# Performance work log

Measured on AMD Instinct MI355X. Metric: run time of the kernel, lower is better.

The kernel has to match this reference:

```python
import jax, jax.numpy as jnp
import numpy as np
from jax import lax

N = 25600      # total nodes = G * T
E = 204800     # edges (before self loops)
IN_CH = 6
HID = 64
HEADS = 4
G = 512        # graphs per batch
T = 50         # sequence length (node_time in [0, T))
OUT = 30       # prediction_horizon * 3
NEG_SLOPE = 0.2
BN_EPS = 1e-5


def _gat(x, src, dst, W, a_src, a_dst, b, heads, outc):
    # PyG GATConv (concat=True): h = x W reshaped to (N, H, C)
    n = x.shape[0]
    h = (x @ W).reshape(n, heads, outc)
    # edge scores: leaky_relu(a_src . h_src + a_dst . h_dst), softmax over incoming edges of dst
    e = jax.nn.leaky_relu((h * a_src).sum(-1)[src] + (h * a_dst).sum(-1)[dst], NEG_SLOPE)  # (E, H)
    m = jax.ops.segment_max(e, dst, num_segments=n)
    ex = jnp.exp(e - m[dst])
    denom = jax.ops.segment_sum(ex, dst, num_segments=n)
    alpha = ex / denom[dst]
    out = jax.ops.segment_sum(alpha[:, :, None] * h[src], dst, num_segments=n)  # (N, H, C)
    return out.reshape(n, heads * outc) + b


def _bn_eval(x, g, b):
    # BatchNorm in eval with running_mean=0, running_var=1
    return g * (x * (1.0 / np.float32(np.sqrt(1.0 + BN_EPS)))) + b


def setup_inputs() -> dict:
    ks = jax.random.split(jax.random.key(0), 16)
    s = 0.1
    d = {}
    d["x"] = jax.random.normal(ks[0], (N, IN_CH), jnp.float32)
    d["edge_index"] = jax.random.randint(ks[1], (2, E), 0, N)
    idx = jnp.arange(N)
    d["batch"] = idx // T       # each graph has exactly T nodes
    d["node_time"] = idx % T
    d["W1"] = jax.random.normal(ks[2], (IN_CH, HEADS * HID), jnp.float32) * s
    d["att_src1"] = jax.random.normal(ks[3], (HEADS, HID), jnp.float32) * s
    d["att_dst1"] = jax.random.normal(ks[4], (HEADS, HID), jnp.float32) * s
    d["b1"] = jnp.zeros((HEADS * HID,), jnp.float32)
    d["g1"] = jnp.ones((HEADS * HID,), jnp.float32)
    d["be1"] = jnp.zeros((HEADS * HID,), jnp.float32)
    d["W2"] = jax.random.normal(ks[5], (HEADS * HID, HID), jnp.float32) * s
    d["att_src2"] = jax.random.normal(ks[6], (1, HID), jnp.float32) * s
    d["att_dst2"] = jax.random.normal(ks[7], (1, HID), jnp.float32) * s
    d["b2"] = jnp.zeros((HID,), jnp.float32)
    d["g2"] = jnp.ones((HID,), jnp.float32)
    d["be2"] = jnp.zeros((HID,), jnp.float32)
    d["Wih"] = jax.random.normal(ks[8], (4 * HID, HID), jnp.float32) * s
    d["Whh"] = jax.random.normal(ks[9], (4 * HID, HID), jnp.float32) * s
    d["bih"] = jnp.zeros((4 * HID,), jnp.float32)
    d["bhh"] = jnp.zeros((4 * HID,), jnp.float32)
    d["Wfc"] = jax.random.normal(ks[10], (HID, OUT), jnp.float32) * s
    d["bfc"] = jnp.zeros((OUT,), jnp.float32)
    return d


def reference(x, edge_index, batch, node_time, W1, att_src1, att_dst1, b1, g1, be1,
              W2, att_src2, att_dst2, b2, g2, be2, Wih, Whh, bih, bhh, Wfc, bfc):
    loops = jnp.arange(N)
    src = jnp.concatenate([edge_index[0], loops])  # GATConv adds self loops
    dst = jnp.concatenate([edge_index[1], loops])
    h = jax.nn.elu(_bn_eval(_gat(x, src, dst, W1, att_src1, att_dst1, b1, HEADS, HID), g1, be1))
    h = jax.nn.elu(_bn_eval(_gat(h, src, dst, W2, att_src2, att_dst2, b2, 1, HID), g2, be2))
    # vectorized replacement of the per-node python scatter loop
    x_seq = jnp.zeros((G, T, HID), h.dtype).at[batch, node_time].set(h)

    def step(carry, xt):
        hh, cc = carry
        gates = xt @ Wih.T + bih + hh @ Whh.T + bhh
        i, f, gg, o = jnp.split(gates, 4, axis=-1)
        cc = jax.nn.sigmoid(f) * cc + jax.nn.sigmoid(i) * jnp.tanh(gg)
        hh = jax.nn.sigmoid(o) * jnp.tanh(cc)
        return (hh, cc), None

    init = (jnp.zeros((G, HID), h.dtype), jnp.zeros((G, HID), h.dtype))
    (hn, _), _ = lax.scan(step, init, x_seq.transpose(1, 0, 2))  # scan over time
    return hn @ Wfc + bfc  # (G, 30)
```

## Files before the change

### kernel.cpp

```cpp
#include <hip/hip_runtime.h>

#define N_NODES 25600
#define N_EDGES 204800
#define EE (N_EDGES + N_NODES)
#define IN_CH 6
#define HID 64
#define HEADS 4
#define G_GRAPHS 512
#define T_STEPS 50
#define OUT_DIM 30
#define NEG_SLOPE 0.2f
#define BN_INV 0.9999950000374997f

__device__ __forceinline__ float lrelu_(float x){ return x > 0.f ? x : NEG_SLOPE * x; }
__device__ __forceinline__ float elu_(float x){ return x > 0.f ? x : __expf(x) - 1.f; }
__device__ __forceinline__ float sigmoid_(float x){ return 1.f / (1.f + __expf(-x)); }

__global__ void count_k(const int* __restrict__ ei, int* __restrict__ counts){
    int e = blockIdx.x * 256 + threadIdx.x;
    if (e >= EE) return;
    int dst = (e < N_EDGES) ? ei[N_EDGES + e] : (e - N_EDGES);
    atomicAdd(&counts[dst], 1);
}

__global__ void scan_k(const int* __restrict__ counts, int* __restrict__ row_ptr,
                       int* __restrict__ cursor){
    __shared__ int part[1024];
    int t = threadIdx.x;
    const int CH = N_NODES / 1024;
    int base = t * CH;
    int s = 0;
    for (int i = 0; i < CH; i++) s += counts[base + i];
    part[t] = s;
    __syncthreads();
    for (int off = 1; off < 1024; off <<= 1){
        int v = (t >= off) ? part[t - off] : 0;
        __syncthreads();
        part[t] += v;
        __syncthreads();
    }
    int run = (t > 0) ? part[t - 1] : 0;
    for (int i = 0; i < CH; i++){
        int cv = counts[base + i];
        row_ptr[base + i] = run;
        cursor[base + i]  = run;
        run += cv;
    }
    if (t == 1023) row_ptr[N_NODES] = run;
}

__global__ void scatter_k(const int* __restrict__ ei, int* __restrict__ cursor,
                          int* __restrict__ ssrc){
    int e = blockIdx.x * 256 + threadIdx.x;
    if (e >= EE) return;
    int src, dst;
    if (e < N_EDGES){ src = ei[e]; dst = ei[N_EDGES + e]; }
    else            { src = dst = e - N_EDGES; }
    int pos = atomicAdd(&cursor[dst], 1);
    ssrc[pos] = src;
}

__global__ void gat1_tr(const float* __restrict__ x, const float* __restrict__ W1,
                        const float* __restrict__ asw, const float* __restrict__ adw,
                        float* __restrict__ h1_pre, float* __restrict__ as1,
                        float* __restrict__ ad1){
    __shared__ float w[IN_CH * 256];
    int tid = threadIdx.x;
    for (int i = tid; i < IN_CH * 256; i += 256) w[i] = W1[i];
    __syncthreads();
    int wv = tid >> 6, lane = tid & 63;
    int n = blockIdx.x * 4 + wv;
    float xv[IN_CH];
    #pragma unroll
    for (int k = 0; k < IN_CH; k++) xv[k] = x[n * IN_CH + k];
    float sA[4], sD[4];
    #pragma unroll
    for (int h = 0; h < 4; h++){
        int col = h * 64 + lane;
        float acc = 0.f;
        #pragma unroll
        for (int k = 0; k < IN_CH; k++) acc += xv[k] * w[k * 256 + col];
        h1_pre[n * 256 + col] = acc;
        sA[h] = acc * asw[col];
        sD[h] = acc * adw[col];
    }
    #pragma unroll
    for (int h = 0; h < 4; h++){
        #pragma unroll
        for (int off = 32; off; off >>= 1){
            sA[h] += __shfl_xor(sA[h], off);
            sD[h] += __shfl_xor(sD[h], off);
        }
    }
    if (lane == 0){
        *(float4*)&as1[n * 4] = make_float4(sA[0], sA[1], sA[2], sA[3]);
        *(float4*)&ad1[n * 4] = make_float4(sD[0], sD[1], sD[2], sD[3]);
    }
}

__global__ void gat1_agg(const float* __restrict__ h1_pre, const float* __restrict__ as1,
                         const float* __restrict__ ad1, const int* __restrict__ row_ptr,
                         const int* __restrict__ ssrc,
                         const float* __restrict__ b1, const float* __restrict__ g1,
                         const float* __restrict__ be1, float* __restrict__ h1_act){
    int wv = threadIdx.x >> 6, lane = threadIdx.x & 63;
    int n = blockIdx.x * 4 + wv;
    int s0 = row_ptr[n], s1 = row_ptr[n + 1];
    float4 adn = *(const float4*)&ad1[n * 4];
    float d0 = 0.f, d1 = 0.f, d2 = 0.f, d3 = 0.f;
    float a0 = 0.f, a1 = 0.f, a2 = 0.f, a3 = 0.f;
    for (int j = s0; j < s1; j++){
        int s = ssrc[j];
        float4 as = *(const float4*)&as1[s * 4];
        float e0 = __expf(lrelu_(as.x + adn.x));
        float e1 = __expf(lrelu_(as.y + adn.y));
        float e2 = __expf(lrelu_(as.z + adn.z));
        float e3 = __expf(lrelu_(as.w + adn.w));
        d0 += e0; d1 += e1; d2 += e2; d3 += e3;
        const float* hp = h1_pre + (size_t)s * 256;
        a0 += e0 * hp[lane];
        a1 += e1 * hp[64 + lane];
        a2 += e2 * hp[128 + lane];
        a3 += e3 * hp[192 + lane];
    }
    float accs[4] = {a0 / d0, a1 / d1, a2 / d2, a3 / d3};
    #pragma unroll
    for (int h = 0; h < 4; h++){
        int col = h * 64 + lane;
        float v = accs[h] + b1[col];
        v = g1[col] * (v * BN_INV) + be1[col];
        h1_act[(size_t)n * 256 + col] = elu_(v);
    }
}

#define TM 64
#define KT 32
#define APAD 4
__global__ __launch_bounds__(256) void gat2_tr(const float* __restrict__ h1_act,
                        const float* __restrict__ W2,
                        const float* __restrict__ asw, const float* __restrict__ adw,
                        float* __restrict__ h2_pre, float* __restrict__ as2,
                        float* __restrict__ ad2){
    __shared__ float As[TM][KT + APAD];
    __shared__ float Bs[KT][64];
    int tx = threadIdx.x;
    int rg = tx >> 4;
    int cg = tx & 15;
    int r0 = rg * 4, c0 = cg * 4;
    int rowBase = blockIdx.x * TM;
    float acc[4][4] = {};
    for (int k0 = 0; k0 < 256; k0 += KT){
        #pragma unroll
        for (int it = 0; it < 2; it++){
            int i = tx + it * 256;
            int row = i >> 3;
            int c4  = (i & 7) * 4;
            *(float4*)&As[row][c4] =
                *(const float4*)(h1_act + (size_t)(rowBase + row) * 256 + k0 + c4);
        }
        #pragma unroll
        for (int it = 0; it < 2; it++){
            int i = tx + it * 256;
            int row = i >> 4;
            int c4  = (i & 15) * 4;
            *(float4*)&Bs[row][c4] = *(const float4*)(W2 + (size_t)(k0 + row) * 64 + c4);
        }
        __syncthreads();
        #pragma unroll
        for (int kq = 0; kq < KT; kq += 4){
            float4 b0 = *(float4*)&Bs[kq + 0][c0];
            float4 b1v = *(float4*)&Bs[kq + 1][c0];
            float4 b2v = *(float4*)&Bs[kq + 2][c0];
            float4 b3 = *(float4*)&Bs[kq + 3][c0];
            #pragma unroll
            for (int i = 0; i < 4; i++){
                float4 a = *(float4*)&As[r0 + i][kq];
                acc[i][0] += a.x * b0.x + a.y * b1v.x + a.z * b2v.x + a.w * b3.x;
                acc[i][1] += a.x * b0.y + a.y * b1v.y + a.z * b2v.y + a.w * b3.y;
                acc[i][2] += a.x * b0.z + a.y * b1v.z + a.z * b2v.z + a.w * b3.z;
                acc[i][3] += a.x * b0.w + a.y * b1v.w + a.z * b2v.w + a.w * b3.w;
            }
        }
        __syncthreads();
    }
    float aw0 = asw[c0], aw1 = asw[c0+1], aw2 = asw[c0+2], aw3 = asw[c0+3];
    float dw0 = adw[c0], dw1 = adw[c0+1], dw2 = adw[c0+2], dw3 = adw[c0+3];
    #pragma unroll
    for (int i = 0; i < 4; i++){
        int row = rowBase + r0 + i;
        *(float4*)(h2_pre + (size_t)row * 64 + c0) =
            make_float4(acc[i][0], acc[i][1], acc[i][2], acc[i][3]);
        float sA = acc[i][0]*aw0 + acc[i][1]*aw1 + acc[i][2]*aw2 + acc[i][3]*aw3;
        float sD = acc[i][0]*dw0 + acc[i][1]*dw1 + acc[i][2]*dw2 + acc[i][3]*dw3;
        #pragma unroll
        for (int off = 8; off; off >>= 1){
            sA += __shfl_xor(sA, off);
            sD += __shfl_xor(sD, off);
        }
        if (cg == 0){ as2[row] = sA; ad2[row] = sD; }
    }
}

__global__ void gat2_agg(const float* __restrict__ h2_pre, const float* __restrict__ as2,
                         const float* __restrict__ ad2, const int* __restrict__ row_ptr,
                         const int* __restrict__ ssrc,
                         const float* __restrict__ b2, const float* __restrict__ g2,
                         const float* __restrict__ be2,
                         const int* __restrict__ batch, const int* __restrict__ ntime,
                         float* __restrict__ xseq){
    int wv = threadIdx.x >> 6, lane = threadIdx.x & 63;
    int n = blockIdx.x * 4 + wv;
    int s0 = row_ptr[n], s1 = row_ptr[n + 1];
    float adn = ad2[n];
    float denom = 0.f, acc = 0.f;
    for (int j = s0; j < s1; j++){
        int s = ssrc[j];
        float e = __expf(lrelu_(as2[s] + adn));
        denom += e;
        acc += e * h2_pre[(size_t)s * 64 + lane];
    }
    float v = acc / denom + b2[lane];
    v = g2[lane] * (v * BN_INV) + be2[lane];
    v = elu_(v);
    int pos = batch[n] * T_STEPS + ntime[n];
    xseq[(size_t)pos * 64 + lane] = v;
}

__global__ __launch_bounds__(256, 2) void lstm_k(const float* __restrict__ xseq,
        const float* __restrict__ Wih, const float* __restrict__ Whh,
        const float* __restrict__ bih, const float* __restrict__ bhh,
        const float* __restrict__ Wfc, const float* __restrict__ bfc,
        float* __restrict__ out){
    int g = blockIdx.x;
    int j = threadIdx.x;
    __shared__ float4 xt4[16];
    __shared__ float4 h4[16];
    __shared__ float gates[256];
    float4 wih[16], whh[16];
    const float4* Wr = (const float4*)(Wih + j * 64);
    const float4* Hr = (const float4*)(Whh + j * 64);
    #pragma unroll
    for (int k = 0; k < 16; k++){ wih[k] = Wr[k]; whh[k] = Hr[k]; }
    float bsum = bih[j] + bhh[j];
    float c = 0.f;
    if (j < 16) h4[j] = make_float4(0.f, 0.f, 0.f, 0.f);
    __syncthreads();
    const float4* xg = (const float4*)(xseq + (size_t)g * T_STEPS * 64);
    for (int t = 0; t < T_STEPS; t++){
        if (j < 16) xt4[j] = xg[t * 16 + j];
        __syncthreads();
        float acc = bsum;
        #pragma unroll
        for (int k = 0; k < 16; k++){
            float4 xv = xt4[k]; float4 wv = wih[k];
            acc += wv.x * xv.x; acc += wv.y * xv.y;
            acc += wv.z * xv.z; acc += wv.w * xv.w;
            float4 hv = h4[k]; float4 wh = whh[k];
            acc += wh.x * hv.x; acc += wh.y * hv.y;
            acc += wh.z * hv.z; acc += wh.w * hv.w;
        }
        gates[j] = acc;
        __syncthreads();
        if (j < 64){
            float iv = gates[j], fv = gates[64 + j], gv = gates[128 + j], ov = gates[192 + j];
            c = sigmoid_(fv) * c + sigmoid_(iv) * tanhf(gv);
            float hn = sigmoid_(ov) * tanhf(c);
            ((float*)h4)[j] = hn;
        }
        __syncthreads();
    }
    if (j < OUT_DIM){
        float acc = bfc[j];
        const float* hf = (const float*)h4;
        #pragma unroll
        for (int k = 0; k < 64; k++) acc += hf[k] * Wfc[k * OUT_DIM + j];
        out[g * OUT_DIM + j] = acc;
    }
}

extern "C" void kernel_launch(void* const* d_in, const int* in_sizes, int n_in,
                              void* d_out, int out_size, void* d_ws, size_t ws_size,
                              hipStream_t stream){
    const float* x    = (const float*)d_in[0];
    const int*   ei   = (const int*)  d_in[1];
    const int*   batch= (const int*)  d_in[2];
    const int*   ntime= (const int*)  d_in[3];
    const float* W1   = (const float*)d_in[4];
    const float* as1w = (const float*)d_in[5];
    const float* ad1w = (const float*)d_in[6];
    const float* b1   = (const float*)d_in[7];
    const float* g1   = (const float*)d_in[8];
    const float* be1  = (const float*)d_in[9];
    const float* W2   = (const float*)d_in[10];
    const float* as2w = (const float*)d_in[11];
    const float* ad2w = (const float*)d_in[12];
    const float* b2   = (const float*)d_in[13];
    const float* g2   = (const float*)d_in[14];
    const float* be2  = (const float*)d_in[15];
    const float* Wih  = (const float*)d_in[16];
    const float* Whh  = (const float*)d_in[17];
    const float* bih  = (const float*)d_in[18];
    const float* bhh  = (const float*)d_in[19];
    const float* Wfc  = (const float*)d_in[20];
    const float* bfc  = (const float*)d_in[21];
    float* out = (float*)d_out;

    char* w = (char*)d_ws;
    auto alloc = [&](size_t bytes)->char*{
        char* p = w;
        w += (bytes + 255) & ~size_t(255);
        return p;
    };
    float* h1_pre = (float*)alloc((size_t)N_NODES * 256 * 4);
    float* h1_act = (float*)alloc((size_t)N_NODES * 256 * 4);
    float* h2_pre = (float*)alloc((size_t)N_NODES * 64 * 4);
    float* xseq   = (float*)alloc((size_t)G_GRAPHS * T_STEPS * 64 * 4);
    float* as1    = (float*)alloc((size_t)N_NODES * 4 * 4);
    float* ad1    = (float*)alloc((size_t)N_NODES * 4 * 4);
    float* as2    = (float*)alloc((size_t)N_NODES * 4);
    float* ad2    = (float*)alloc((size_t)N_NODES * 4);
    int* counts   = (int*)alloc((size_t)N_NODES * 4);
    int* row_ptr  = (int*)alloc((size_t)(N_NODES + 1) * 4);
    int* cursor   = (int*)alloc((size_t)N_NODES * 4);
    int* ssrc     = (int*)alloc((size_t)EE * 4);

    hipMemsetAsync(counts, 0, (size_t)N_NODES * 4, stream);
    count_k  <<<(EE + 255) / 256, 256, 0, stream>>>(ei, counts);
    scan_k   <<<1, 1024, 0, stream>>>(counts, row_ptr, cursor);
    scatter_k<<<(EE + 255) / 256, 256, 0, stream>>>(ei, cursor, ssrc);
    gat1_tr  <<<N_NODES / 4, 256, 0, stream>>>(x, W1, as1w, ad1w, h1_pre, as1, ad1);
    gat1_agg <<<N_NODES / 4, 256, 0, stream>>>(h1_pre, as1, ad1, row_ptr, ssrc, b1, g1, be1, h1_act);
    gat2_tr  <<<N_NODES / TM, 256, 0, stream>>>(h1_act, W2, as2w, ad2w, h2_pre, as2, ad2);
    gat2_agg <<<N_NODES / 4, 256, 0, stream>>>(h2_pre, as2, ad2, row_ptr, ssrc, b2, g2, be2, batch, ntime, xseq);
    lstm_k   <<<G_GRAPHS, 256, 0, stream>>>(xseq, Wih, Whh, bih, bhh, Wfc, bfc, out);
}
```

Baseline: 318.8 us.

## Hoist LSTM input projection into a batched GEMM and streamline recurrence

The input-to-hidden LSTM projection for all timesteps is computed up front in a new tiled GEMM kernel (gx_k) that writes into the reused h1_pre buffer. The recurrent kernel then only does the hidden-to-hidden matvec, broadcasting h across lanes with readlane instead of shared memory. Gates are double-buffered so each step needs one barrier instead of three, and sigmoid and tanh use fast reciprocal forms. The cost is an extra launch and a global write and read of the gate preactivations, plus slightly less accurate activations.

```diff
diff --git a/kernel.cpp b/kernel.cpp
--- a/kernel.cpp
+++ b/kernel.cpp
@@ -14,7 +14,15 @@
 
 __device__ __forceinline__ float lrelu_(float x){ return x > 0.f ? x : NEG_SLOPE * x; }
 __device__ __forceinline__ float elu_(float x){ return x > 0.f ? x : __expf(x) - 1.f; }
-__device__ __forceinline__ float sigmoid_(float x){ return 1.f / (1.f + __expf(-x)); }
+__device__ __forceinline__ float sigmoid_(float x){
+    return __builtin_amdgcn_rcpf(1.f + __expf(-x));
+}
+__device__ __forceinline__ float tanh_(float x){
+    return 1.f - 2.f * __builtin_amdgcn_rcpf(1.f + __expf(2.f * x));
+}
+__device__ __forceinline__ float bcast_(float v, int l){
+    return __int_as_float(__builtin_amdgcn_readlane(__float_as_int(v), l));
+}
 
 __global__ void count_k(const int* __restrict__ ei, int* __restrict__ counts){
     int e = blockIdx.x * 256 + threadIdx.x;
@@ -226,54 +234,107 @@
     xseq[(size_t)pos * 64 + lane] = v;
 }
 
-__global__ __launch_bounds__(256, 2) void lstm_k(const float* __restrict__ xseq,
-        const float* __restrict__ Wih, const float* __restrict__ Whh,
-        const float* __restrict__ bih, const float* __restrict__ bhh,
+__global__ __launch_bounds__(256) void gx_k(const float* __restrict__ xseq,
+        const float* __restrict__ Wih, const float* __restrict__ bih,
+        const float* __restrict__ bhh, float* __restrict__ gx){
+    __shared__ float As[64][68];
+    __shared__ float Bs[64][128];
+    int tx = threadIdx.x;
+    int rowBase = blockIdx.x * 64;
+    int colBase = blockIdx.y * 128;
+    #pragma unroll
+    for (int it = 0; it < 4; it++){
+        int i = tx + it * 256;
+        int r = i >> 4;
+        int c4 = (i & 15) * 4;
+        *(float4*)&As[r][c4] = *(const float4*)(xseq + (size_t)(rowBase + r) * 64 + c4);
+    }
+    #pragma unroll
+    for (int it = 0; it < 8; it++){
+        int i = tx + it * 256;
+        int jj = i & 127;
+        int k4 = (i >> 7) * 4;
+        float4 wv = *(const float4*)(Wih + (size_t)(colBase + jj) * 64 + k4);
+        Bs[k4 + 0][jj] = wv.x;
+        Bs[k4 + 1][jj] = wv.y;
+        Bs[k4 + 2][jj] = wv.z;
+        Bs[k4 + 3][jj] = wv.w;
+    }
+    __syncthreads();
+    int rg = tx >> 5;
+    int cg = tx & 31;
+    int r0 = rg * 8, c0 = cg * 4;
+    float acc[8][4] = {};
+    #pragma unroll
+    for (int kq = 0; kq < 64; kq += 4){
+        float4 b0 = *(float4*)&Bs[kq + 0][c0];
+        float4 b1 = *(float4*)&Bs[kq + 1][c0];
+        float4 b2 = *(float4*)&Bs[kq + 2][c0];
+        float4 b3 = *(float4*)&Bs[kq + 3][c0];
+        #pragma unroll
+        for (int i = 0; i < 8; i++){
+            float4 a = *(float4*)&As[r0 + i][kq];
+            acc[i][0] += a.x * b0.x + a.y * b1.x + a.z * b2.x + a.w * b3.x;
+            acc[i][1] += a.x * b0.y + a.y * b1.y + a.z * b2.y + a.w * b3.y;
+            acc[i][2] += a.x * b0.z + a.y * b1.z + a.z * b2.z + a.w * b3.z;
+            acc[i][3] += a.x * b0.w + a.y * b1.w + a.z * b2.w + a.w * b3.w;
+        }
+    }
+    int col = colBase + c0;
+    float4 bb = make_float4(bih[col] + bhh[col], bih[col+1] + bhh[col+1],
+                            bih[col+2] + bhh[col+2], bih[col+3] + bhh[col+3]);
+    #pragma unroll
+    for (int i = 0; i < 8; i++){
+        int row = rowBase + r0 + i;
+        *(float4*)(gx + (size_t)row * 256 + col) =
+            make_float4(acc[i][0] + bb.x, acc[i][1] + bb.y,
+                        acc[i][2] + bb.z, acc[i][3] + bb.w);
+    }
+}
+
+__global__ __launch_bounds__(256, 2) void lstm_k(const float* __restrict__ gx,
+        const float* __restrict__ Whh,
         const float* __restrict__ Wfc, const float* __restrict__ bfc,
         float* __restrict__ out){
     int g = blockIdx.x;
     int j = threadIdx.x;
-    __shared__ float4 xt4[16];
-    __shared__ float4 h4[16];
-    __shared__ float gates[256];
-    float4 wih[16], whh[16];
-    const float4* Wr = (const float4*)(Wih + j * 64);
+    int lane = j & 63;
+    __shared__ float gates[2][256];
+    float4 whh[16];
     const float4* Hr = (const float4*)(Whh + j * 64);
     #pragma unroll
-    for (int k = 0; k < 16; k++){ wih[k] = Wr[k]; whh[k] = Hr[k]; }
-    float bsum = bih[j] + bhh[j];
-    float c = 0.f;
-    if (j < 16) h4[j] = make_float4(0.f, 0.f, 0.f, 0.f);
+    for (int k = 0; k < 16; k++) whh[k] = Hr[k];
+    float h = 0.f, c = 0.f;
+    const float* gxg = gx + (size_t)g * T_STEPS * 256;
+    float gxv = gxg[j];
+    for (int t = 0; t < T_STEPS; t++){
+        float gx_next = (t + 1 < T_STEPS) ? gxg[(t + 1) * 256 + j] : 0.f;
+        float a0 = gxv, a1 = 0.f, a2 = 0.f, a3 = 0.f;
+        #pragma unroll
+        for (int k = 0; k < 16; k++){
+            float4 wv = whh[k];
+            a0 += wv.x * bcast_(h, 4 * k + 0);
+            a1 += wv.y * bcast_(h, 4 * k + 1);
+            a2 += wv.z * bcast_(h, 4 * k + 2);
+            a3 += wv.w * bcast_(h, 4 * k + 3);
+        }
+        int buf = t & 1;
+        gates[buf][j] = (a0 + a1) + (a2 + a3);
+        __syncthreads();
+        float iv = gates[buf][lane];
+        float fv = gates[buf][64 + lane];
+        float gv = gates[buf][128 + lane];
+        float ov = gates[buf][192 + lane];
+        c = sigmoid_(fv) * c + sigmoid_(iv) * tanh_(gv);
+        h = sigmoid_(ov) * tanh_(c);
+        gxv = gx_next;
+    }
+    if (j < 64) gates[0][j] = h;
     __syncthreads();
-    const float4* xg = (const float4*)(xseq + (size_t)g * T_STEPS * 64);
-    for (int t = 0; t < T_STEPS; t++){
-        if (j < 16) xt4[j] = xg[t * 16 + j];
-        __syncthreads();
-        float acc = bsum;
-        #pragma unroll
-        for (int k = 0; k < 16; k++){
-            float4 xv = xt4[k]; float4 wv = wih[k];
-            acc += wv.x * xv.x; acc += wv.y * xv.y;
-            acc += wv.z * xv.z; acc += wv.w * xv.w;
-            float4 hv = h4[k]; float4 wh = whh[k];
-            acc += wh.x * hv.x; acc += wh.y * hv.y;
-            acc += wh.z * hv.z; acc += wh.w * hv.w;
-        }
-        gates[j] = acc;
-        __syncthreads();
-        if (j < 64){
-            float iv = gates[j], fv = gates[64 + j], gv = gates[128 + j], ov = gates[192 + j];
-            c = sigmoid_(fv) * c + sigmoid_(iv) * tanhf(gv);
-            float hn = sigmoid_(ov) * tanhf(c);
-            ((float*)h4)[j] = hn;
-        }
-        __syncthreads();
-    }
     if (j < OUT_DIM){
         float acc = bfc[j];
-        const float* hf = (const float*)h4;
-        #pragma unroll
-        for (int k = 0; k < 64; k++) acc += hf[k] * Wfc[k * OUT_DIM + j];
+        #pragma unroll
+        for (int k = 0; k < 64; k++) acc += gates[0][k] * Wfc[k * OUT_DIM + j];
         out[g * OUT_DIM + j] = acc;
     }
 }
@@ -323,6 +384,7 @@
     int* row_ptr  = (int*)alloc((size_t)(N_NODES + 1) * 4);
     int* cursor   = (int*)alloc((size_t)N_NODES * 4);
     int* ssrc     = (int*)alloc((size_t)EE * 4);
+    float* gx     = h1_pre;
 
     hipMemsetAsync(counts, 0, (size_t)N_NODES * 4, stream);
     count_k  <<<(EE + 255) / 256, 256, 0, stream>>>(ei, counts);
@@ -332,5 +394,6 @@
     gat1_agg <<<N_NODES / 4, 256, 0, stream>>>(h1_pre, as1, ad1, row_ptr, ssrc, b1, g1, be1, h1_act);
     gat2_tr  <<<N_NODES / TM, 256, 0, stream>>>(h1_act, W2, as2w, ad2w, h2_pre, as2, ad2);
     gat2_agg <<<N_NODES / 4, 256, 0, stream>>>(h2_pre, as2, ad2, row_ptr, ssrc, b2, g2, be2, batch, ntime, xseq);
-    lstm_k   <<<G_GRAPHS, 256, 0, stream>>>(xseq, Wih, Whh, bih, bhh, Wfc, bfc, out);
-}
+    gx_k     <<<dim3(N_NODES / 64, 2), 256, 0, stream>>>(xseq, Wih, bih, bhh, gx);
+    lstm_k   <<<G_GRAPHS, 256, 0, stream>>>(gx, Whh, Wfc, bfc, out);
+}
```

New measurement: 318.3 us. Within noise of the previous version (-0.2%).
